# Kernel optimization log

Hardware: AMD Instinct MI355X
Metric: run time of the kernel (lower is better)

Reference implementation:

```python
import jax, jax.numpy as jnp
import numpy as np

BIN_AGG = 2  # binAgg in binFunc

def pair_mean(x):
    # mean over non-overlapping groups of BIN_AGG along last dim, then repeat back
    B, C, H, W = x.shape
    m = x.reshape(B, C, H, W // BIN_AGG, BIN_AGG).mean(axis=-1)  # [B,C,H,W/2]
    return jnp.repeat(m, BIN_AGG, axis=-1)  # [B,C,H,W]

def bin_active(x):
    # binFunc(x, abs_bin=True) * sign(x): per-pair mean of |x| carrying the sign of x
    return pair_mean(jnp.abs(x)) * jnp.sign(x)

def setup_inputs() -> dict:
    key = jax.random.key(0)
    k1, k2, k3 = jax.random.split(key, 3)
    Cin, Cout, K = 256, 256, 3
    x = jax.random.normal(k1, (32, Cin, 56, 56), jnp.float32)
    bound = 1.0 / np.sqrt(Cin * K * K)  # torch Conv2d default init range
    weight = jax.random.uniform(k2, (Cout, Cin, K, K), jnp.float32, -bound, bound)
    bias = jax.random.uniform(k3, (Cout,), jnp.float32, -bound, bound)
    return {"x": x, "weight": weight, "bias": bias}

def reference(x, weight, bias):
    xb = bin_active(x)
    out = jax.lax.conv_general_dilated(
        xb, weight, window_strides=(1, 1), padding=[(1, 1), (1, 1)],
        dimension_numbers=("NCHW", "OIHW", "NCHW"))
    return out + bias[None, :, None, None]
```

## Files before the change

kernel.cpp:

```cpp
#include <hip/hip_runtime.h>
#include <hip/hip_bf16.h>
#include <cstdint>

typedef unsigned short u16;
typedef __attribute__((ext_vector_type(8))) short short8;
typedef __attribute__((ext_vector_type(4))) float f32x4;

#define NB   32
#define CIN  256
#define HH   56
#define WWID 56
#define HP   58
#define WP   58
#define COUT 256
#define NSPAT (NB*HH*WWID)

__device__ __forceinline__ u16 f2bf(float f) {
  uint32_t u = __float_as_uint(f);
  u += 0x7FFFu + ((u >> 16) & 1u);
  return (u16)(u >> 16);
}

__device__ __forceinline__ void gload16(const void* g, void* lds) {
  auto* gp = reinterpret_cast<const __attribute__((address_space(1))) uint32_t*>(
      reinterpret_cast<uintptr_t>(g));
  auto* lp = reinterpret_cast<__attribute__((address_space(3))) uint32_t*>(
      reinterpret_cast<uintptr_t>(lds));
  __builtin_amdgcn_global_load_lds(gp, lp, 16, 0, 0);
}

__global__ __launch_bounds__(256) void prep_x_kernel(const float* __restrict__ x,
                                                     u16* __restrict__ xbp) {
  const int n = blockIdx.x, hp = blockIdx.y, t = threadIdx.x;
  u16* row = xbp + ((size_t)(n*HP + hp))*WP*CIN;
  if (hp == 0 || hp == HP-1) {
    uint32_t* p = (uint32_t*)row;
    for (int i = t; i < WP*CIN/2; i += 256) p[i] = 0;
    return;
  }
  const int h = hp - 1;
  __shared__ u16 lds[CIN*15*4];
  if (t < 224) {
    const int f4 = t % 14, c0 = t / 14;
    #pragma unroll
    for (int ci = 0; ci < 16; ci++) {
      const int c = c0*16 + ci;
      const float4 v = *(const float4*)(x + (((size_t)n*CIN + c)*HH + h)*WWID + f4*4);
      const float m01 = 0.5f*(fabsf(v.x)+fabsf(v.y));
      const float m23 = 0.5f*(fabsf(v.z)+fabsf(v.w));
      ushort4 o;
      o.x = f2bf(v.x == 0.f ? 0.f : copysignf(m01, v.x));
      o.y = f2bf(v.y == 0.f ? 0.f : copysignf(m01, v.y));
      o.z = f2bf(v.z == 0.f ? 0.f : copysignf(m23, v.z));
      o.w = f2bf(v.w == 0.f ? 0.f : copysignf(m23, v.w));
      *(ushort4*)&lds[(c*15 + f4)*4] = o;
    }
  }
  __syncthreads();
  if (t < 128) {
    ((uint32_t*)row)[t] = 0;
    ((uint32_t*)(row + (WP-1)*CIN))[t] = 0;
    const int c0 = 2*t;
    #pragma unroll
    for (int w = 0; w < WWID; w++) {
      const uint32_t u0 = lds[(c0*15 + (w>>2))*4 + (w&3)];
      const uint32_t u1 = lds[((c0+1)*15 + (w>>2))*4 + (w&3)];
      ((uint32_t*)(row + (w+1)*CIN))[t] = u0 | (u1 << 16);
    }
  }
}

__global__ __launch_bounds__(256) void prep_w_kernel(const float* __restrict__ wsrc,
                                                     u16* __restrict__ wr) {
  const int idx = blockIdx.x*256 + threadIdx.x;
  const int co = idx >> 8, ci = idx & 255;
  const float* s = wsrc + (size_t)idx*9;
  #pragma unroll
  for (int p = 0; p < 9; p++)
    wr[((size_t)p*COUT + co)*CIN + ci] = f2bf(s[p]);
}

__global__ __launch_bounds__(256) void conv_kernel(const u16* __restrict__ xbp,
                                                   const u16* __restrict__ wr,
                                                   const float* __restrict__ bias,
                                                   float* __restrict__ out) {
  __shared__ u16 ldsA[128*64];
  __shared__ u16 ldsB[128*64];
  const int t = threadIdx.x;
  const int wv = t >> 6, l = t & 63;
  const int mtile = blockIdx.x, ntile = blockIdx.y;

  const int cs8 = (((l & 7) ^ (l >> 3)) << 3);
  const int rb  = wv*8 + (l >> 3);

  int base0[4];
  #pragma unroll
  for (int i = 0; i < 4; i++) {
    const int m  = mtile*128 + i*32 + rb;
    const int n  = m / 3136, hw = m % 3136;
    base0[i] = ((n*HP + hw/WWID)*WP + (hw%WWID))*CIN;
  }

  f32x4 acc[4][4];
  #pragma unroll
  for (int a = 0; a < 4; a++)
    #pragma unroll
    for (int b = 0; b < 4; b++) {
      acc[a][b][0] = 0.f; acc[a][b][1] = 0.f; acc[a][b][2] = 0.f; acc[a][b][3] = 0.f;
    }

  for (int ks = 0; ks < 36; ks++) {
    const int pos = ks >> 2, cb = ks & 3;
    const int posoff = ((pos/3)*WP + (pos%3))*CIN;
    const int koff = cb*64 + cs8;
    #pragma unroll
    for (int i = 0; i < 4; i++) {
      const u16* gA = wr + (((pos*COUT + ntile*128 + i*32 + rb) << 8) + koff);
      gload16(gA, &ldsA[(i*4 + wv)*512]);
      const u16* gB = xbp + base0[i] + posoff + koff;
      gload16(gB, &ldsB[(i*4 + wv)*512]);
    }
    __syncthreads();
    #pragma unroll
    for (int kk = 0; kk < 2; kk++) {
      const int ch = (l >> 4) + 4*kk;
      short8 af[4], bfr[4];
      #pragma unroll
      for (int mi = 0; mi < 4; mi++) {
        const int r = (wv & 1)*64 + mi*16 + (l & 15);
        af[mi] = *(const short8*)&ldsA[r*64 + ((ch ^ (r & 7)) << 3)];
      }
      #pragma unroll
      for (int ni = 0; ni < 4; ni++) {
        const int r = (wv >> 1)*64 + ni*16 + (l & 15);
        bfr[ni] = *(const short8*)&ldsB[r*64 + ((ch ^ (r & 7)) << 3)];
      }
      #pragma unroll
      for (int mi = 0; mi < 4; mi++)
        #pragma unroll
        for (int ni = 0; ni < 4; ni++)
          acc[mi][ni] = __builtin_amdgcn_mfma_f32_16x16x32_bf16(af[mi], bfr[ni], acc[mi][ni], 0, 0, 0);
    }
    __syncthreads();
  }

  const int co0 = ntile*128 + (wv & 1)*64 + ((l >> 4) << 2);
  float bi[4][4];
  #pragma unroll
  for (int mi = 0; mi < 4; mi++)
    #pragma unroll
    for (int j = 0; j < 4; j++)
      bi[mi][j] = bias[co0 + mi*16 + j];
  const int mb = mtile*128 + (wv >> 1)*64 + (l & 15);
  #pragma unroll
  for (int ni = 0; ni < 4; ni++) {
    const int m = mb + ni*16;
    const int n = m / 3136, hw = m % 3136;
    float* orow = out + (size_t)n*COUT*3136 + hw;
    #pragma unroll
    for (int mi = 0; mi < 4; mi++) {
      #pragma unroll
      for (int j = 0; j < 4; j++)
        orow[(size_t)(co0 + mi*16 + j)*3136] = acc[mi][ni][j] + bi[mi][j];
    }
  }
}

extern "C" void kernel_launch(void* const* d_in, const int* in_sizes, int n_in,
                              void* d_out, int out_size, void* d_ws, size_t ws_size,
                              hipStream_t stream) {
  const float* x      = (const float*)d_in[0];
  const float* weight = (const float*)d_in[1];
  const float* bias   = (const float*)d_in[2];
  float* out = (float*)d_out;

  u16* xbp = (u16*)d_ws;
  u16* wrr = xbp + (size_t)NB*HP*WP*CIN;

  prep_x_kernel<<<dim3(NB, HP), 256, 0, stream>>>(x, xbp);
  prep_w_kernel<<<dim3(256), 256, 0, stream>>>(weight, wrr);
  conv_kernel<<<dim3(NSPAT/128, 2), 256, 0, stream>>>(xbp, wrr, bias, out);
}
```

Before: 373.5 us.

## Double-buffer conv LDS loads, remap blocks across XCDs, vectorize prep transpose

The conv kernel now double-buffers its A/B LDS tiles so the global-to-LDS loads for the next K step are issued before the MFMAs on the current step. This is meant to hide load latency, at the cost of twice the LDS footprint and possibly lower occupancy. The grid is flattened to one dimension and block IDs are remapped so neighbouring tiles land on the same XCD, for better L2 reuse. The prep_x transpose uses a swizzled channel-major LDS layout with 16-byte vector stores and spreads the writes over all 256 threads.

```diff
diff --git a/kernel.cpp b/kernel.cpp
--- a/kernel.cpp
+++ b/kernel.cpp
@@ -39,34 +39,36 @@
     return;
   }
   const int h = hp - 1;
-  __shared__ u16 lds[CIN*15*4];
+  __shared__ u16 lds[HH*CIN];
   if (t < 224) {
-    const int f4 = t % 14, c0 = t / 14;
+    const int f4 = t % 14, c0 = (t / 14) * 16;
+    const int sw = f4 & 7;
     #pragma unroll
     for (int ci = 0; ci < 16; ci++) {
-      const int c = c0*16 + ci;
+      const int c = c0 + ci;
       const float4 v = *(const float4*)(x + (((size_t)n*CIN + c)*HH + h)*WWID + f4*4);
       const float m01 = 0.5f*(fabsf(v.x)+fabsf(v.y));
       const float m23 = 0.5f*(fabsf(v.z)+fabsf(v.w));
-      ushort4 o;
-      o.x = f2bf(v.x == 0.f ? 0.f : copysignf(m01, v.x));
-      o.y = f2bf(v.y == 0.f ? 0.f : copysignf(m01, v.y));
-      o.z = f2bf(v.z == 0.f ? 0.f : copysignf(m23, v.z));
-      o.w = f2bf(v.w == 0.f ? 0.f : copysignf(m23, v.w));
-      *(ushort4*)&lds[(c*15 + f4)*4] = o;
+      u16 o[4];
+      o[0] = f2bf(v.x == 0.f ? 0.f : copysignf(m01, v.x));
+      o[1] = f2bf(v.y == 0.f ? 0.f : copysignf(m01, v.y));
+      o[2] = f2bf(v.z == 0.f ? 0.f : copysignf(m23, v.z));
+      o[3] = f2bf(v.w == 0.f ? 0.f : copysignf(m23, v.w));
+      const int cs = ((((c >> 3) ^ sw) & 31) << 3) | (c & 7);
+      #pragma unroll
+      for (int j = 0; j < 4; j++)
+        lds[(f4*4 + j)*CIN + cs] = o[j];
     }
   }
   __syncthreads();
-  if (t < 128) {
-    ((uint32_t*)row)[t] = 0;
-    ((uint32_t*)(row + (WP-1)*CIN))[t] = 0;
-    const int c0 = 2*t;
-    #pragma unroll
-    for (int w = 0; w < WWID; w++) {
-      const uint32_t u0 = lds[(c0*15 + (w>>2))*4 + (w&3)];
-      const uint32_t u1 = lds[((c0+1)*15 + (w>>2))*4 + (w&3)];
-      ((uint32_t*)(row + (w+1)*CIN))[t] = u0 | (u1 << 16);
-    }
+  if (t < 128) ((uint32_t*)row)[t] = 0;
+  else ((uint32_t*)(row + (WP-1)*CIN))[t-128] = 0;
+  #pragma unroll
+  for (int it = 0; it < 7; it++) {
+    const int q = it*256 + t;
+    const int w = q >> 5, ck = q & 31;
+    const short8 v = *(const short8*)&lds[w*CIN + ((ck ^ ((w >> 2) & 7)) << 3)];
+    *(short8*)(row + (size_t)(w+1)*CIN + (ck << 3)) = v;
   }
 }
 
@@ -84,11 +86,13 @@
                                                    const u16* __restrict__ wr,
                                                    const float* __restrict__ bias,
                                                    float* __restrict__ out) {
-  __shared__ u16 ldsA[128*64];
-  __shared__ u16 ldsB[128*64];
+  __shared__ u16 ldsA[2][128*64];
+  __shared__ u16 ldsB[2][128*64];
   const int t = threadIdx.x;
   const int wv = t >> 6, l = t & 63;
-  const int mtile = blockIdx.x, ntile = blockIdx.y;
+  const int bid = blockIdx.x;
+  const int b9 = (bid & 7)*196 + (bid >> 3);
+  const int ntile = b9 & 1, mtile = b9 >> 1;
 
   const int cs8 = (((l & 7) ^ (l >> 3)) << 3);
   const int rb  = wv*8 + (l >> 3);
@@ -101,6 +105,19 @@
     base0[i] = ((n*HP + hw/WWID)*WP + (hw%WWID))*CIN;
   }
 
+  auto STAGE = [&](int buf, int ks) {
+    const int pos = ks >> 2, cb = ks & 3;
+    const int posoff = ((pos/3)*WP + (pos%3))*CIN;
+    const int koff = cb*64 + cs8;
+    #pragma unroll
+    for (int i = 0; i < 4; i++) {
+      const u16* gA = wr + (((pos*COUT + ntile*128 + i*32 + rb) << 8) + koff);
+      gload16(gA, &ldsA[buf][(i*4 + wv)*512]);
+      const u16* gB = xbp + base0[i] + posoff + koff;
+      gload16(gB, &ldsB[buf][(i*4 + wv)*512]);
+    }
+  };
+
   f32x4 acc[4][4];
   #pragma unroll
   for (int a = 0; a < 4; a++)
@@ -109,18 +126,11 @@
       acc[a][b][0] = 0.f; acc[a][b][1] = 0.f; acc[a][b][2] = 0.f; acc[a][b][3] = 0.f;
     }
 
+  STAGE(0, 0);
+  __syncthreads();
+  int cur = 0;
   for (int ks = 0; ks < 36; ks++) {
-    const int pos = ks >> 2, cb = ks & 3;
-    const int posoff = ((pos/3)*WP + (pos%3))*CIN;
-    const int koff = cb*64 + cs8;
-    #pragma unroll
-    for (int i = 0; i < 4; i++) {
-      const u16* gA = wr + (((pos*COUT + ntile*128 + i*32 + rb) << 8) + koff);
-      gload16(gA, &ldsA[(i*4 + wv)*512]);
-      const u16* gB = xbp + base0[i] + posoff + koff;
-      gload16(gB, &ldsB[(i*4 + wv)*512]);
-    }
-    __syncthreads();
+    if (ks < 35) STAGE(cur ^ 1, ks + 1);
     #pragma unroll
     for (int kk = 0; kk < 2; kk++) {
       const int ch = (l >> 4) + 4*kk;
@@ -128,12 +138,12 @@
       #pragma unroll
       for (int mi = 0; mi < 4; mi++) {
         const int r = (wv & 1)*64 + mi*16 + (l & 15);
-        af[mi] = *(const short8*)&ldsA[r*64 + ((ch ^ (r & 7)) << 3)];
+        af[mi] = *(const short8*)&ldsA[cur][r*64 + ((ch ^ (r & 7)) << 3)];
       }
       #pragma unroll
       for (int ni = 0; ni < 4; ni++) {
         const int r = (wv >> 1)*64 + ni*16 + (l & 15);
-        bfr[ni] = *(const short8*)&ldsB[r*64 + ((ch ^ (r & 7)) << 3)];
+        bfr[ni] = *(const short8*)&ldsB[cur][r*64 + ((ch ^ (r & 7)) << 3)];
       }
       #pragma unroll
       for (int mi = 0; mi < 4; mi++)
@@ -142,6 +152,7 @@
           acc[mi][ni] = __builtin_amdgcn_mfma_f32_16x16x32_bf16(af[mi], bfr[ni], acc[mi][ni], 0, 0, 0);
     }
     __syncthreads();
+    cur ^= 1;
   }
 
   const int co0 = ntile*128 + (wv & 1)*64 + ((l >> 4) << 2);
@@ -179,5 +190,5 @@
 
   prep_x_kernel<<<dim3(NB, HP), 256, 0, stream>>>(x, xbp);
   prep_w_kernel<<<dim3(256), 256, 0, stream>>>(weight, wrr);
-  conv_kernel<<<dim3(NSPAT/128, 2), 256, 0, stream>>>(xbp, wrr, bias, out);
+  conv_kernel<<<dim3(NSPAT/128 * 2), 256, 0, stream>>>(xbp, wrr, bias, out);
 }
```

Result: faster. 334.1 us (-10.5%).
